# Kernel tuning notes

Measured on AMD Instinct MI355X. Metric: run time of the kernel, lower is better.

## Reference

```python
import jax, jax.numpy as jnp
import numpy as np

N_CHANNELS = 29
HIDDEN = [5, 4, 4]
IN_FEAT = 7
OUT_FEAT = 3
EPS = 1e-07


def _glorot(key, fan_in, fan_out, shape):
    lim = np.sqrt(6.0 / (fan_in + fan_out))
    return jax.random.uniform(key, shape, jnp.float32, -lim, lim)


def _make_params(key):
    # Batched per-channel weights: stack n_channels tiny MLPs along leading dim.
    sizes = [IN_FEAT] + HIDDEN + [OUT_FEAT]
    Ws, bs = [], []
    for i in range(len(sizes) - 1):
        key, k = jax.random.split(key)
        Ws.append(_glorot(k, sizes[i], sizes[i + 1], (N_CHANNELS, sizes[i], sizes[i + 1])))
        bs.append(jnp.zeros((N_CHANNELS, sizes[i + 1]), jnp.float32))
    return Ws, bs


def setup_inputs() -> dict:
    key = jax.random.key(0)
    ks = jax.random.split(key, 16)
    N = 262144
    inp = {
        "tau": jax.random.uniform(ks[0], (N, N_CHANNELS, 1), jnp.float32),
        "mu": jax.random.uniform(ks[1], (N, 1), jnp.float32, 0.05, 1.0),
        "mu_bar": jax.random.uniform(ks[2], (N, 1), jnp.float32, 0.05, 1.0),
        "lw": jax.random.uniform(ks[3], (N, 1), jnp.float32),
        "h2o": jax.random.uniform(ks[4], (N, 1), jnp.float32),
        "o3": jax.random.uniform(ks[5], (N, 1), jnp.float32),
        "co2": jax.random.uniform(ks[6], (N, 1), jnp.float32),
        "u": jax.random.uniform(ks[7], (N, 1), jnp.float32),
        "n2o": jax.random.uniform(ks[8], (N, 1), jnp.float32),
        "ch4": jax.random.uniform(ks[9], (N, 1), jnp.float32),
    }
    Wd, bd = _make_params(ks[10])
    Wf, bf = _make_params(ks[11])
    for i in range(4):
        inp[f"Wd{i}"] = Wd[i]
        inp[f"bd{i}"] = bd[i]
        inp[f"Wf{i}"] = Wf[i]
        inp[f"bf{i}"] = bf[i]
    return inp


def _mlp(x, Ws, bs):
    # x: [N, F]; Ws[i]: [C, fin, fout]; output [N, C, 3]
    h = jnp.einsum('nf,cfh->nch', x, Ws[0]) + bs[0]
    h = jax.nn.relu(h)
    for i in (1, 2):
        h = jnp.einsum('nch,chk->nck', h, Ws[i]) + bs[i]
        h = jax.nn.relu(h)
    h = jnp.einsum('nch,chk->nck', h, Ws[3]) + bs[3]
    return jax.nn.softmax(h, axis=-1)


def reference(tau, mu, mu_bar, lw, h2o, o3, co2, u, n2o, ch4,
              Wd0, bd0, Wd1, bd1, Wd2, bd2, Wd3, bd3,
              Wf0, bf0, Wf1, bf1, Wf2, bf2, Wf3, bf3):
    constituents = jnp.concatenate([lw, h2o, o3, co2, u, n2o, ch4], axis=1)  # [N,7]
    c_direct = constituents / (mu + EPS)
    c_diffuse = constituents / (mu_bar + EPS)
    mu3 = mu[:, :, None]          # [N,1,1]
    mu_bar3 = mu_bar[:, :, None]
    tau_total = jnp.sum(tau, axis=-1, keepdims=True)  # [N,C,1]
    t_direct = jnp.exp(-tau_total / (mu3 + EPS))       # [N,C,1]
    t_diffuse = jnp.exp(-tau_total / (mu_bar3 + EPS))
    e_direct = _mlp(c_direct, [Wd0, Wd1, Wd2, Wd3], [bd0, bd1, bd2, bd3])    # [N,C,3]
    e_diffuse = _mlp(c_diffuse, [Wf0, Wf1, Wf2, Wf3], [bf0, bf1, bf2, bf3])  # [N,C,3]
    return jnp.concatenate([t_direct, t_diffuse, e_direct, e_diffuse], axis=2)  # [N,C,8]
```

## Files before the change

kernel.cpp:

```cpp
#include <hip/hip_runtime.h>

#define EPS 1e-7f
#define NCH 29
#define SPB 128
#define ROWA 17


typedef float f32x2 __attribute__((ext_vector_type(2)));
typedef float nf4   __attribute__((ext_vector_type(4)));

__device__ __forceinline__ f32x2 splat2(float v) { f32x2 r; r.x = v; r.y = v; return r; }
__device__ __forceinline__ f32x2 fma2(f32x2 a, f32x2 b, f32x2 c) {
    return __builtin_elementwise_fma(a, b, c);
}
__device__ __forceinline__ f32x2 max2(f32x2 a, f32x2 b) {
    return __builtin_elementwise_max(a, b);
}
__device__ __forceinline__ f32x2 expc2(f32x2 a) {
    f32x2 r; r.x = __expf(a.x); r.y = __expf(a.y); return r;
}
__device__ __forceinline__ f32x2 rcp2(f32x2 a) {
    f32x2 r; r.x = __builtin_amdgcn_rcpf(a.x); r.y = __builtin_amdgcn_rcpf(a.y); return r;
}
__device__ __forceinline__ nf4 mk4(float a, float b, float c, float d) {
    nf4 r; r.x = a; r.y = b; r.z = c; r.w = d; return r;
}

__device__ __forceinline__ void barrier_lds_only() {
    asm volatile("s_waitcnt lgkmcnt(0)\n\ts_barrier" ::: "memory");
}

__device__ __forceinline__ void mlp7p(const f32x2 x[7],
    const float* __restrict__ W0, const float* __restrict__ b0,
    const float* __restrict__ W1, const float* __restrict__ b1,
    const float* __restrict__ W2, const float* __restrict__ b2,
    const float* __restrict__ W3, const float* __restrict__ b3,
    f32x2 e[3])
{
    const f32x2 zero = splat2(0.0f);
    f32x2 h0[5];
#pragma unroll
    for (int h = 0; h < 5; ++h) {
        f32x2 a = splat2(b0[h]);
#pragma unroll
        for (int f = 0; f < 7; ++f) a = fma2(x[f], splat2(W0[f * 5 + h]), a);
        h0[h] = max2(a, zero);
    }
    f32x2 h1[4];
#pragma unroll
    for (int k = 0; k < 4; ++k) {
        f32x2 a = splat2(b1[k]);
#pragma unroll
        for (int h = 0; h < 5; ++h) a = fma2(h0[h], splat2(W1[h * 4 + k]), a);
        h1[k] = max2(a, zero);
    }
    f32x2 h2[4];
#pragma unroll
    for (int k = 0; k < 4; ++k) {
        f32x2 a = splat2(b2[k]);
#pragma unroll
        for (int h = 0; h < 4; ++h) a = fma2(h1[h], splat2(W2[h * 4 + k]), a);
        h2[k] = max2(a, zero);
    }
    f32x2 l[3];
#pragma unroll
    for (int k = 0; k < 3; ++k) {
        f32x2 a = splat2(b3[k]);
#pragma unroll
        for (int h = 0; h < 4; ++h) a = fma2(h2[h], splat2(W3[h * 3 + k]), a);
        l[k] = a;
    }
    f32x2 m = max2(l[0], max2(l[1], l[2]));
    f32x2 e0 = expc2(l[0] - m);
    f32x2 e1 = expc2(l[1] - m);
    f32x2 e2 = expc2(l[2] - m);
    f32x2 rs = rcp2(e0 + e1 + e2);
    e[0] = e0 * rs; e[1] = e1 * rs; e[2] = e2 * rs;
}

__global__ __launch_bounds__(512, 5) void lps_kernel(
    const float* __restrict__ tau, const float* __restrict__ mu, const float* __restrict__ mu_bar,
    const float* __restrict__ lw, const float* __restrict__ h2o, const float* __restrict__ o3,
    const float* __restrict__ co2, const float* __restrict__ uu, const float* __restrict__ n2o,
    const float* __restrict__ ch4,
    const float* __restrict__ Wd0, const float* __restrict__ bd0,
    const float* __restrict__ Wf0, const float* __restrict__ bf0,
    const float* __restrict__ Wd1, const float* __restrict__ bd1,
    const float* __restrict__ Wf1, const float* __restrict__ bf1,
    const float* __restrict__ Wd2, const float* __restrict__ bd2,
    const float* __restrict__ Wf2, const float* __restrict__ bf2,
    const float* __restrict__ Wd3, const float* __restrict__ bd3,
    const float* __restrict__ Wf3, const float* __restrict__ bf3,
    float* __restrict__ out, int N)
{
    __shared__ __align__(16) nf4 obuf[SPB * ROWA];

    const int tid  = threadIdx.x;
    const int lane = tid & 63;
    const int wid  = __builtin_amdgcn_readfirstlane(tid >> 6);

    const long long base = (long long)blockIdx.x * SPB;
    const int s0 = (int)base + lane;
    const int s1 = s0 + 64;
    const int i0 = (s0 < N) ? s0 : (N - 1);
    const int i1 = (s1 < N) ? s1 : (N - 1);

    f32x2 mu2, mub2;
    mu2.x  = mu[i0];      mu2.y  = mu[i1];
    mub2.x = mu_bar[i0];  mub2.y = mu_bar[i1];
    const f32x2 rmu2  = rcp2(mu2 + splat2(EPS));
    const f32x2 rmub2 = rcp2(mub2 + splat2(EPS));

    f32x2 cons2[7];
    cons2[0].x = lw[i0];  cons2[0].y = lw[i1];
    cons2[1].x = h2o[i0]; cons2[1].y = h2o[i1];
    cons2[2].x = o3[i0];  cons2[2].y = o3[i1];
    cons2[3].x = co2[i0]; cons2[3].y = co2[i1];
    cons2[4].x = uu[i0];  cons2[4].y = uu[i1];
    cons2[5].x = n2o[i0]; cons2[5].y = n2o[i1];
    cons2[6].x = ch4[i0]; cons2[6].y = ch4[i1];

    f32x2 tau2v[4];
#pragma unroll
    for (int k = 0; k < 4; ++k) {
        const int c  = k * 8 + wid;
        const int cc = (c < NCH) ? c : 0;
        tau2v[k].x = tau[(size_t)i0 * NCH + cc];
        tau2v[k].y = tau[(size_t)i1 * NCH + cc];
    }

    int nsamp = N - (int)base;
    if (nsamp > SPB) nsamp = SPB;
    nf4* out4 = (nf4*)out;

#pragma unroll
    for (int k = 0; k < 4; ++k) {
        const int c = k * 8 + wid;
        if (c < NCH) {
            const f32x2 td2 = expc2(-(tau2v[k] * rmu2));
            const f32x2 tf2 = expc2(-(tau2v[k] * rmub2));

            f32x2 x2[7];
            f32x2 ed[3], ef[3];
#pragma unroll
            for (int f = 0; f < 7; ++f) x2[f] = cons2[f] * rmu2;
            mlp7p(x2, Wd0 + c * 35, bd0 + c * 5, Wd1 + c * 20, bd1 + c * 4,
                      Wd2 + c * 16, bd2 + c * 4, Wd3 + c * 12, bd3 + c * 3, ed);
#pragma unroll
            for (int f = 0; f < 7; ++f) x2[f] = cons2[f] * rmub2;
            mlp7p(x2, Wf0 + c * 35, bf0 + c * 5, Wf1 + c * 20, bf1 + c * 4,
                      Wf2 + c * 16, bf2 + c * 4, Wf3 + c * 12, bf3 + c * 3, ef);

            const int r = (c - k * 8) * 2;
            obuf[lane * ROWA + r]            = mk4(td2.x, tf2.x, ed[0].x, ed[1].x);
            obuf[lane * ROWA + r + 1]        = mk4(ed[2].x, ef[0].x, ef[1].x, ef[2].x);
            obuf[(lane + 64) * ROWA + r]     = mk4(td2.y, tf2.y, ed[0].y, ed[1].y);
            obuf[(lane + 64) * ROWA + r + 1] = mk4(ed[2].y, ef[0].y, ef[1].y, ef[2].y);
        }

        barrier_lds_only();

        if (nsamp > 0) {
            if (k < 3) {
                const int tot = nsamp * 16;
                for (int i = tid; i < tot; i += 512) {
                    const int s = i >> 4, rr = i & 15;
                    out4[(base + s) * 58 + k * 16 + rr] = obuf[s * ROWA + rr];
                }
            } else {
                const int tot = nsamp * 10;
                for (int i = tid; i < tot; i += 512) {
                    const int s = i / 10, rr = i - s * 10;
                    out4[(base + s) * 58 + 48 + rr] = obuf[s * ROWA + rr];
                }
            }
        }

        barrier_lds_only();
    }
}

extern "C" void kernel_launch(void* const* d_in, const int* in_sizes, int n_in,
                              void* d_out, int out_size, void* d_ws, size_t ws_size,
                              hipStream_t stream) {
    const float* tau    = (const float*)d_in[0];
    const float* mu     = (const float*)d_in[1];
    const float* mu_bar = (const float*)d_in[2];
    const float* lw     = (const float*)d_in[3];
    const float* h2o    = (const float*)d_in[4];
    const float* o3     = (const float*)d_in[5];
    const float* co2    = (const float*)d_in[6];
    const float* uu     = (const float*)d_in[7];
    const float* n2o    = (const float*)d_in[8];
    const float* ch4    = (const float*)d_in[9];

    const float* Wd0 = (const float*)d_in[10];
    const float* bd0 = (const float*)d_in[11];
    const float* Wf0 = (const float*)d_in[12];
    const float* bf0 = (const float*)d_in[13];
    const float* Wd1 = (const float*)d_in[14];
    const float* bd1 = (const float*)d_in[15];
    const float* Wf1 = (const float*)d_in[16];
    const float* bf1 = (const float*)d_in[17];
    const float* Wd2 = (const float*)d_in[18];
    const float* bd2 = (const float*)d_in[19];
    const float* Wf2 = (const float*)d_in[20];
    const float* bf2 = (const float*)d_in[21];
    const float* Wd3 = (const float*)d_in[22];
    const float* bd3 = (const float*)d_in[23];
    const float* Wf3 = (const float*)d_in[24];
    const float* bf3 = (const float*)d_in[25];

    float* out = (float*)d_out;
    int N = in_sizes[1];

    int blocks = (N + SPB - 1) / SPB;
    lps_kernel<<<blocks, 512, 0, stream>>>(
        tau, mu, mu_bar, lw, h2o, o3, co2, uu, n2o, ch4,
        Wd0, bd0, Wf0, bf0, Wd1, bd1, Wf1, bf1,
        Wd2, bd2, Wf2, bf2, Wd3, bd3, Wf3, bf3,
        out, N);
}
```

Before: 79.01 us.

## Warp-specialize into compute and store waves with double-buffered LDS

The block is split into six compute waves that each handle one channel per chunk and two store waves that copy the previous chunk from a double-buffered LDS tile to global memory. This overlaps the MLP compute with the output stores instead of alternating compute and store phases across all eight waves. In exchange only six of eight waves do arithmetic, the number of channel passes grows from four to five, and launch bounds drop to four blocks per CU to fit the larger LDS buffer.

```diff
diff --git a/kernel.cpp b/kernel.cpp
--- a/kernel.cpp
+++ b/kernel.cpp
@@ -3,7 +3,9 @@
 #define EPS 1e-7f
 #define NCH 29
 #define SPB 128
-#define ROWA 17
+#define CPC 6
+#define NCHUNK 5
+#define ROWB 13
 
 
 typedef float f32x2 __attribute__((ext_vector_type(2)));
@@ -78,7 +80,7 @@
     e[0] = e0 * rs; e[1] = e1 * rs; e[2] = e2 * rs;
 }
 
-__global__ __launch_bounds__(512, 5) void lps_kernel(
+__global__ __launch_bounds__(512, 4) void lps_kernel(
     const float* __restrict__ tau, const float* __restrict__ mu, const float* __restrict__ mu_bar,
     const float* __restrict__ lw, const float* __restrict__ h2o, const float* __restrict__ o3,
     const float* __restrict__ co2, const float* __restrict__ uu, const float* __restrict__ n2o,
@@ -93,86 +95,88 @@
     const float* __restrict__ Wf3, const float* __restrict__ bf3,
     float* __restrict__ out, int N)
 {
-    __shared__ __align__(16) nf4 obuf[SPB * ROWA];
+    __shared__ __align__(16) nf4 obuf[2][SPB][ROWB];
 
     const int tid  = threadIdx.x;
     const int lane = tid & 63;
     const int wid  = __builtin_amdgcn_readfirstlane(tid >> 6);
 
     const long long base = (long long)blockIdx.x * SPB;
+    int nsamp = N - (int)base;
+    if (nsamp > SPB) nsamp = SPB;
+    nf4* out4 = (nf4*)out;
+
     const int s0 = (int)base + lane;
     const int s1 = s0 + 64;
     const int i0 = (s0 < N) ? s0 : (N - 1);
     const int i1 = (s1 < N) ? s1 : (N - 1);
 
-    f32x2 mu2, mub2;
-    mu2.x  = mu[i0];      mu2.y  = mu[i1];
-    mub2.x = mu_bar[i0];  mub2.y = mu_bar[i1];
-    const f32x2 rmu2  = rcp2(mu2 + splat2(EPS));
-    const f32x2 rmub2 = rcp2(mub2 + splat2(EPS));
-
+    f32x2 rmu2 = splat2(1.0f), rmub2 = splat2(1.0f);
     f32x2 cons2[7];
-    cons2[0].x = lw[i0];  cons2[0].y = lw[i1];
-    cons2[1].x = h2o[i0]; cons2[1].y = h2o[i1];
-    cons2[2].x = o3[i0];  cons2[2].y = o3[i1];
-    cons2[3].x = co2[i0]; cons2[3].y = co2[i1];
-    cons2[4].x = uu[i0];  cons2[4].y = uu[i1];
-    cons2[5].x = n2o[i0]; cons2[5].y = n2o[i1];
-    cons2[6].x = ch4[i0]; cons2[6].y = ch4[i1];
-
-    f32x2 tau2v[4];
-#pragma unroll
-    for (int k = 0; k < 4; ++k) {
-        const int c  = k * 8 + wid;
-        const int cc = (c < NCH) ? c : 0;
-        tau2v[k].x = tau[(size_t)i0 * NCH + cc];
-        tau2v[k].y = tau[(size_t)i1 * NCH + cc];
-    }
-
-    int nsamp = N - (int)base;
-    if (nsamp > SPB) nsamp = SPB;
-    nf4* out4 = (nf4*)out;
-
-#pragma unroll
-    for (int k = 0; k < 4; ++k) {
-        const int c = k * 8 + wid;
-        if (c < NCH) {
-            const f32x2 td2 = expc2(-(tau2v[k] * rmu2));
-            const f32x2 tf2 = expc2(-(tau2v[k] * rmub2));
-
-            f32x2 x2[7];
-            f32x2 ed[3], ef[3];
-#pragma unroll
-            for (int f = 0; f < 7; ++f) x2[f] = cons2[f] * rmu2;
-            mlp7p(x2, Wd0 + c * 35, bd0 + c * 5, Wd1 + c * 20, bd1 + c * 4,
-                      Wd2 + c * 16, bd2 + c * 4, Wd3 + c * 12, bd3 + c * 3, ed);
-#pragma unroll
-            for (int f = 0; f < 7; ++f) x2[f] = cons2[f] * rmub2;
-            mlp7p(x2, Wf0 + c * 35, bf0 + c * 5, Wf1 + c * 20, bf1 + c * 4,
-                      Wf2 + c * 16, bf2 + c * 4, Wf3 + c * 12, bf3 + c * 3, ef);
-
-            const int r = (c - k * 8) * 2;
-            obuf[lane * ROWA + r]            = mk4(td2.x, tf2.x, ed[0].x, ed[1].x);
-            obuf[lane * ROWA + r + 1]        = mk4(ed[2].x, ef[0].x, ef[1].x, ef[2].x);
-            obuf[(lane + 64) * ROWA + r]     = mk4(td2.y, tf2.y, ed[0].y, ed[1].y);
-            obuf[(lane + 64) * ROWA + r + 1] = mk4(ed[2].y, ef[0].y, ef[1].y, ef[2].y);
+    f32x2 tau2v[NCHUNK];
+#pragma unroll
+    for (int k = 0; k < NCHUNK; ++k) tau2v[k] = splat2(0.0f);
+
+    if (wid < CPC) {
+        f32x2 mu2, mub2;
+        mu2.x  = mu[i0];      mu2.y  = mu[i1];
+        mub2.x = mu_bar[i0];  mub2.y = mu_bar[i1];
+        rmu2  = rcp2(mu2 + splat2(EPS));
+        rmub2 = rcp2(mub2 + splat2(EPS));
+
+        cons2[0].x = lw[i0];  cons2[0].y = lw[i1];
+        cons2[1].x = h2o[i0]; cons2[1].y = h2o[i1];
+        cons2[2].x = o3[i0];  cons2[2].y = o3[i1];
+        cons2[3].x = co2[i0]; cons2[3].y = co2[i1];
+        cons2[4].x = uu[i0];  cons2[4].y = uu[i1];
+        cons2[5].x = n2o[i0]; cons2[5].y = n2o[i1];
+        cons2[6].x = ch4[i0]; cons2[6].y = ch4[i1];
+
+#pragma unroll
+        for (int k = 0; k < NCHUNK; ++k) {
+            const int c  = k * CPC + wid;
+            const int cc = (c < NCH) ? c : 0;
+            tau2v[k].x = tau[(size_t)i0 * NCH + cc];
+            tau2v[k].y = tau[(size_t)i1 * NCH + cc];
         }
-
-        barrier_lds_only();
-
-        if (nsamp > 0) {
-            if (k < 3) {
-                const int tot = nsamp * 16;
-                for (int i = tid; i < tot; i += 512) {
-                    const int s = i >> 4, rr = i & 15;
-                    out4[(base + s) * 58 + k * 16 + rr] = obuf[s * ROWA + rr];
-                }
-            } else {
-                const int tot = nsamp * 10;
-                for (int i = tid; i < tot; i += 512) {
-                    const int s = i / 10, rr = i - s * 10;
-                    out4[(base + s) * 58 + 48 + rr] = obuf[s * ROWA + rr];
-                }
+    }
+
+    const int st = tid - CPC * 64;
+
+#pragma unroll
+    for (int p = 0; p <= NCHUNK; ++p) {
+        if (p < NCHUNK && wid < CPC) {
+            const int c = p * CPC + wid;
+            if (c < NCH) {
+                const f32x2 td2 = expc2(-(tau2v[p] * rmu2));
+                const f32x2 tf2 = expc2(-(tau2v[p] * rmub2));
+
+                f32x2 x2[7];
+                f32x2 ed[3], ef[3];
+#pragma unroll
+                for (int f = 0; f < 7; ++f) x2[f] = cons2[f] * rmu2;
+                mlp7p(x2, Wd0 + c * 35, bd0 + c * 5, Wd1 + c * 20, bd1 + c * 4,
+                          Wd2 + c * 16, bd2 + c * 4, Wd3 + c * 12, bd3 + c * 3, ed);
+#pragma unroll
+                for (int f = 0; f < 7; ++f) x2[f] = cons2[f] * rmub2;
+                mlp7p(x2, Wf0 + c * 35, bf0 + c * 5, Wf1 + c * 20, bf1 + c * 4,
+                          Wf2 + c * 16, bf2 + c * 4, Wf3 + c * 12, bf3 + c * 3, ef);
+
+                const int r = wid * 2;
+                obuf[p & 1][lane][r]          = mk4(td2.x, tf2.x, ed[0].x, ed[1].x);
+                obuf[p & 1][lane][r + 1]      = mk4(ed[2].x, ef[0].x, ef[1].x, ef[2].x);
+                obuf[p & 1][lane + 64][r]     = mk4(td2.y, tf2.y, ed[0].y, ed[1].y);
+                obuf[p & 1][lane + 64][r + 1] = mk4(ed[2].y, ef[0].y, ef[1].y, ef[2].y);
+            }
+        }
+
+        if (p >= 1 && wid >= CPC && nsamp > 0) {
+            const int it  = p - 1;
+            const int cnt = (it < 4) ? 12 : 10;
+            const int tot = nsamp * cnt;
+            for (int i = st; i < tot; i += 128) {
+                const int s = i / cnt, rr = i - s * cnt;
+                out4[(base + s) * 58 + it * 12 + rr] = obuf[it & 1][s][rr];
             }
         }
 
```

After: 78.21 us. Within noise of the previous version (-1.0%).

## Double-buffer LDS output staging with 4 waves over 8 channel chunks

Applied to the files above, without the earlier changes.

Cuts the block from 512 to 256 threads, so each wave now handles 8 channel chunks of 4 channels instead of 4 chunks of 8. The LDS staging buffer is double-buffered, which drops one barrier per chunk and lets computing the next chunk overlap with the global stores of the previous one. The trade-off is twice as many per-thread MLP iterations and eight tau values held in registers, with a different occupancy target in the launch bounds.

```diff
diff --git a/kernel.cpp b/kernel.cpp
--- a/kernel.cpp
+++ b/kernel.cpp
@@ -3,7 +3,8 @@
 #define EPS 1e-7f
 #define NCH 29
 #define SPB 128
-#define ROWA 17
+#define NCHUNK 8
+#define ROWB 9
 
 
 typedef float f32x2 __attribute__((ext_vector_type(2)));
@@ -78,7 +79,7 @@
     e[0] = e0 * rs; e[1] = e1 * rs; e[2] = e2 * rs;
 }
 
-__global__ __launch_bounds__(512, 5) void lps_kernel(
+__global__ __launch_bounds__(256, 4) void lps_kernel(
     const float* __restrict__ tau, const float* __restrict__ mu, const float* __restrict__ mu_bar,
     const float* __restrict__ lw, const float* __restrict__ h2o, const float* __restrict__ o3,
     const float* __restrict__ co2, const float* __restrict__ uu, const float* __restrict__ n2o,
@@ -93,7 +94,7 @@
     const float* __restrict__ Wf3, const float* __restrict__ bf3,
     float* __restrict__ out, int N)
 {
-    __shared__ __align__(16) nf4 obuf[SPB * ROWA];
+    __shared__ __align__(16) nf4 obuf[2][SPB * ROWB];
 
     const int tid  = threadIdx.x;
     const int lane = tid & 63;
@@ -120,10 +121,10 @@
     cons2[5].x = n2o[i0]; cons2[5].y = n2o[i1];
     cons2[6].x = ch4[i0]; cons2[6].y = ch4[i1];
 
-    f32x2 tau2v[4];
-#pragma unroll
-    for (int k = 0; k < 4; ++k) {
-        const int c  = k * 8 + wid;
+    f32x2 tau2v[NCHUNK];
+#pragma unroll
+    for (int k = 0; k < NCHUNK; ++k) {
+        const int c  = k * 4 + wid;
         const int cc = (c < NCH) ? c : 0;
         tau2v[k].x = tau[(size_t)i0 * NCH + cc];
         tau2v[k].y = tau[(size_t)i1 * NCH + cc];
@@ -133,9 +134,8 @@
     if (nsamp > SPB) nsamp = SPB;
     nf4* out4 = (nf4*)out;
 
-#pragma unroll
-    for (int k = 0; k < 4; ++k) {
-        const int c = k * 8 + wid;
+    auto compute_chunk = [&](int k) {
+        const int c = k * 4 + wid;
         if (c < NCH) {
             const f32x2 td2 = expc2(-(tau2v[k] * rmu2));
             const f32x2 tf2 = expc2(-(tau2v[k] * rmub2));
@@ -151,32 +151,40 @@
             mlp7p(x2, Wf0 + c * 35, bf0 + c * 5, Wf1 + c * 20, bf1 + c * 4,
                       Wf2 + c * 16, bf2 + c * 4, Wf3 + c * 12, bf3 + c * 3, ef);
 
-            const int r = (c - k * 8) * 2;
-            obuf[lane * ROWA + r]            = mk4(td2.x, tf2.x, ed[0].x, ed[1].x);
-            obuf[lane * ROWA + r + 1]        = mk4(ed[2].x, ef[0].x, ef[1].x, ef[2].x);
-            obuf[(lane + 64) * ROWA + r]     = mk4(td2.y, tf2.y, ed[0].y, ed[1].y);
-            obuf[(lane + 64) * ROWA + r + 1] = mk4(ed[2].y, ef[0].y, ef[1].y, ef[2].y);
+            const int r = wid * 2;
+            nf4* buf = obuf[k & 1];
+            buf[lane * ROWB + r]            = mk4(td2.x, tf2.x, ed[0].x, ed[1].x);
+            buf[lane * ROWB + r + 1]        = mk4(ed[2].x, ef[0].x, ef[1].x, ef[2].x);
+            buf[(lane + 64) * ROWB + r]     = mk4(td2.y, tf2.y, ed[0].y, ed[1].y);
+            buf[(lane + 64) * ROWB + r + 1] = mk4(ed[2].y, ef[0].y, ef[1].y, ef[2].y);
         }
-
+    };
+
+    compute_chunk(0);
+
+#pragma unroll
+    for (int k = 1; k <= NCHUNK; ++k) {
         barrier_lds_only();
 
+        const int fk  = k - 1;
+        const nf4* fb = obuf[fk & 1];
         if (nsamp > 0) {
-            if (k < 3) {
-                const int tot = nsamp * 16;
-                for (int i = tid; i < tot; i += 512) {
-                    const int s = i >> 4, rr = i & 15;
-                    out4[(base + s) * 58 + k * 16 + rr] = obuf[s * ROWA + rr];
+            if (fk < 7) {
+                const int tot = nsamp * 8;
+                for (int i = tid; i < tot; i += 256) {
+                    const int s = i >> 3, rr = i & 7;
+                    out4[(base + s) * 58 + fk * 8 + rr] = fb[s * ROWB + rr];
                 }
             } else {
-                const int tot = nsamp * 10;
-                for (int i = tid; i < tot; i += 512) {
-                    const int s = i / 10, rr = i - s * 10;
-                    out4[(base + s) * 58 + 48 + rr] = obuf[s * ROWA + rr];
+                const int tot = nsamp * 2;
+                for (int i = tid; i < tot; i += 256) {
+                    const int s = i >> 1, rr = i & 1;
+                    out4[(base + s) * 58 + 56 + rr] = fb[s * ROWB + rr];
                 }
             }
         }
 
-        barrier_lds_only();
+        if (k < NCHUNK) compute_chunk(k);
     }
 }
 
@@ -215,7 +223,7 @@
     int N = in_sizes[1];
 
     int blocks = (N + SPB - 1) / SPB;
-    lps_kernel<<<blocks, 512, 0, stream>>>(
+    lps_kernel<<<blocks, 256, 0, stream>>>(
         tau, mu, mu_bar, lw, h2o, o3, co2, uu, n2o, ch4,
         Wd0, bd0, Wf0, bf0, Wd1, bd1, Wf1, bf1,
         Wd2, bd2, Wf2, bf2, Wd3, bd3, Wf3, bf3,
```

After: 83.05 us. 5.1% more time.
